# Performance work log

Hardware: AMD Instinct MI355X
Metric: run time of the kernel (lower is better)

The kernel has to match this reference:

```python
import jax, jax.numpy as jnp
import numpy as np

NEG_SLOPE = 0.2  # PyG GATConv default negative_slope


def gat_conv(x_src, x_dst, edge_index, W, att_src, att_dst, bias, heads, out_c, concat, num_dst):
    # PyG GATConv (add_self_loops=False, eval mode so dropout is identity).
    # Same shared linear W applied to src and dst (in_channels is an int in PyG).
    h_src = (x_src @ W).reshape(-1, heads, out_c)  # [Ns,H,C]
    h_dst = (x_dst @ W).reshape(-1, heads, out_c)  # [Nd,H,C]
    al_src = jnp.sum(h_src * att_src, axis=-1)     # [Ns,H]
    al_dst = jnp.sum(h_dst * att_dst, axis=-1)     # [Nd,H]
    src, dst = edge_index[0], edge_index[1]
    e = jax.nn.leaky_relu(al_src[src] + al_dst[dst], NEG_SLOPE)  # [E,H]
    # segment softmax over edges sharing the same dst node
    m = jax.ops.segment_max(e, dst, num_segments=num_dst)        # [Nd,H]
    e = jnp.exp(e - m[dst])
    s = jax.ops.segment_sum(e, dst, num_segments=num_dst)        # [Nd,H]
    alpha = e / (s[dst] + 1e-16)                                 # [E,H]
    msg = alpha[:, :, None] * h_src[src]                         # [E,H,C]
    out = jax.ops.segment_sum(msg, dst, num_segments=num_dst)    # [Nd,H,C]
    if concat:
        return out.reshape(num_dst, heads * out_c) + bias
    return out.mean(axis=1) + bias


def setup_inputs() -> dict:
    N, D, HID, H, OUT, E = 50000, 128, 64, 8, 128, 400000
    key = jax.random.key(0)
    ks = jax.random.split(key, 32)
    s = 0.05
    inp = {
        'x_transition': jax.random.normal(ks[0], (N, D), jnp.float32),
        'x_place': jax.random.normal(ks[1], (N, D), jnp.float32),
        'edge_tp': jax.random.randint(ks[2], (2, E), 0, N, jnp.int32),
        'edge_pt': jax.random.randint(ks[3], (2, E), 0, N, jnp.int32),
        # layer 1 (heads=8, concat)
        'W1_tp': jax.random.normal(ks[4], (D, H * HID), jnp.float32) * s,
        'as1_tp': jax.random.normal(ks[5], (H, HID), jnp.float32) * s,
        'ad1_tp': jax.random.normal(ks[6], (H, HID), jnp.float32) * s,
        'b1_tp': jnp.zeros((H * HID,), jnp.float32),
        'W1_pt': jax.random.normal(ks[7], (D, H * HID), jnp.float32) * s,
        'as1_pt': jax.random.normal(ks[8], (H, HID), jnp.float32) * s,
        'ad1_pt': jax.random.normal(ks[9], (H, HID), jnp.float32) * s,
        'b1_pt': jnp.zeros((H * HID,), jnp.float32),
        # layer 2 (heads=1, concat=False)
        'W2_tp': jax.random.normal(ks[10], (H * HID, HID), jnp.float32) * s,
        'as2_tp': jax.random.normal(ks[11], (1, HID), jnp.float32) * s,
        'ad2_tp': jax.random.normal(ks[12], (1, HID), jnp.float32) * s,
        'b2_tp': jnp.zeros((HID,), jnp.float32),
        'W2_pt': jax.random.normal(ks[13], (H * HID, HID), jnp.float32) * s,
        'as2_pt': jax.random.normal(ks[14], (1, HID), jnp.float32) * s,
        'ad2_pt': jax.random.normal(ks[15], (1, HID), jnp.float32) * s,
        'b2_pt': jnp.zeros((HID,), jnp.float32),
        # output linears per node type
        'Wo_t': jax.random.normal(ks[16], (HID, OUT), jnp.float32) * s,
        'bo_t': jnp.zeros((OUT,), jnp.float32),
        'Wo_p': jax.random.normal(ks[17], (HID, OUT), jnp.float32) * s,
        'bo_p': jnp.zeros((OUT,), jnp.float32),
    }
    return inp


def reference(x_transition, x_place, edge_tp, edge_pt,
              W1_tp, as1_tp, ad1_tp, b1_tp, W1_pt, as1_pt, ad1_pt, b1_pt,
              W2_tp, as2_tp, ad2_tp, b2_tp, W2_pt, as2_pt, ad2_pt, b2_pt,
              Wo_t, bo_t, Wo_p, bo_p):
    Nt, Np = x_transition.shape[0], x_place.shape[0]
    H, HID = as1_tp.shape
    # conv1: transition -> place and place -> transition (HeteroConv aggr='sum',
    # each dst type receives exactly one edge type here)
    p1 = gat_conv(x_transition, x_place, edge_tp, W1_tp, as1_tp, ad1_tp, b1_tp, H, HID, True, Np)
    t1 = gat_conv(x_place, x_transition, edge_pt, W1_pt, as1_pt, ad1_pt, b1_pt, H, HID, True, Nt)
    p1, t1 = jax.nn.relu(p1), jax.nn.relu(t1)
    # conv2: heads=1, concat=False
    p2 = gat_conv(t1, p1, edge_tp, W2_tp, as2_tp, ad2_tp, b2_tp, 1, HID, False, Np)
    t2 = gat_conv(p1, t1, edge_pt, W2_pt, as2_pt, ad2_pt, b2_pt, 1, HID, False, Nt)
    p2, t2 = jax.nn.relu(p2), jax.nn.relu(t2)
    out_t = t2 @ Wo_t + bo_t
    out_p = p2 @ Wo_p + bo_p
    return (out_t, out_p)
```

## Files before the change

### kernel.cpp

```cpp
#include <hip/hip_runtime.h>

#define NEG_SLOPE 0.2f

typedef __attribute__((ext_vector_type(8))) short bf16x8;
typedef __attribute__((ext_vector_type(4))) float f32x4;

__device__ __forceinline__ float bf2f(unsigned short u) {
    return __uint_as_float(((unsigned int)u) << 16);
}
__device__ __forceinline__ unsigned short f2bf(float f) {
    unsigned int x = __float_as_uint(f);
    x += 0x7fffu + ((x >> 16) & 1u);
    return (unsigned short)(x >> 16);
}
__device__ __forceinline__ float ld1(const float* p) { return *p; }
__device__ __forceinline__ float ld1(const unsigned short* p) { return bf2f(*p); }
__device__ __forceinline__ void st1(float* p, float v) { *p = v; }
__device__ __forceinline__ void st1(unsigned short* p, float v) { *p = f2bf(v); }

__global__ void cvt_bf16_kernel(const float* __restrict__ in, unsigned short* __restrict__ out, int n) {
    int i = blockIdx.x * blockDim.x + threadIdx.x;
    if (i < n) out[i] = f2bf(in[i]);
}

__global__ void transpose_cvt_kernel(const float* __restrict__ in, unsigned short* __restrict__ out,
                                     int K, int N) {
    int i = blockIdx.x * blockDim.x + threadIdx.x;
    if (i >= K * N) return;
    int k = i / N, n = i - k * N;
    out[(size_t)n * K + k] = f2bf(in[i]);
}

__global__ void fold1_bt_kernel(const float* __restrict__ W_s, const float* __restrict__ av_s,
                                const float* __restrict__ W_d, const float* __restrict__ av_d,
                                unsigned short* __restrict__ out) {
    int idx = blockIdx.x * blockDim.x + threadIdx.x;
    if (idx >= 16 * 128) return;
    int h = idx >> 7, d = idx & 127;
    const float* W = (h < 8) ? W_s : W_d;
    const float* a = (h < 8) ? (av_s + h * 64) : (av_d + (h - 8) * 64);
    const float* wr = W + (size_t)d * 512 + (h & 7) * 64;
    float s = 0.f;
#pragma unroll
    for (int c = 0; c < 64; ++c) s = fmaf(wr[c], a[c], s);
    out[idx] = f2bf(s);
}

__global__ void fold2_bt_kernel(const float* __restrict__ W_s, const float* __restrict__ av_s,
                                const float* __restrict__ W_d, const float* __restrict__ av_d,
                                unsigned short* __restrict__ out) {
    int idx = blockIdx.x * blockDim.x + threadIdx.x;
    if (idx >= 16 * 512) return;
    int h = idx >> 9, d = idx & 511;
    float s = 0.f;
    if (h < 2) {
        const float* W = (h == 0) ? W_s : W_d;
        const float* a = (h == 0) ? av_s : av_d;
        const float* wr = W + (size_t)d * 64;
#pragma unroll
        for (int c = 0; c < 64; ++c) s = fmaf(wr[c], a[c], s);
    }
    out[idx] = f2bf(s);
}

__global__ void hist_kernel(const int* __restrict__ dst, int E, int* __restrict__ deg) {
    int i = blockIdx.x * blockDim.x + threadIdx.x;
    if (i < E) atomicAdd(&deg[dst[i]], 1);
}

__global__ __launch_bounds__(512) void scan_chunk_kernel(const int* __restrict__ in, int N,
                                                         int* __restrict__ incl, int* __restrict__ sums) {
    __shared__ int sm[512];
    int i = blockIdx.x * 512 + threadIdx.x;
    int v = (i < N) ? in[i] : 0;
    sm[threadIdx.x] = v;
    __syncthreads();
    for (int off = 1; off < 512; off <<= 1) {
        int t = (threadIdx.x >= off) ? sm[threadIdx.x - off] : 0;
        __syncthreads();
        sm[threadIdx.x] += t;
        __syncthreads();
    }
    if (i < N) incl[i] = sm[threadIdx.x];
    if (threadIdx.x == 511) sums[blockIdx.x] = sm[511];
}

__global__ __launch_bounds__(512) void scan_sums_kernel(int* __restrict__ sums, int n) {
    __shared__ int sm[512];
    int v = (threadIdx.x < n) ? sums[threadIdx.x] : 0;
    sm[threadIdx.x] = v;
    __syncthreads();
    for (int off = 1; off < 512; off <<= 1) {
        int t = (threadIdx.x >= off) ? sm[threadIdx.x - off] : 0;
        __syncthreads();
        sm[threadIdx.x] += t;
        __syncthreads();
    }
    if (threadIdx.x < n) sums[threadIdx.x] = sm[threadIdx.x] - v;
}

__global__ void scan_fin_kernel(const int* __restrict__ incl, const int* __restrict__ deg,
                                const int* __restrict__ sums, int N,
                                int* __restrict__ rowptr, int* __restrict__ cursor) {
    int i = blockIdx.x * blockDim.x + threadIdx.x;
    if (i >= N) return;
    int excl = incl[i] - deg[i] + sums[i >> 9];
    rowptr[i] = excl;
    cursor[i] = excl;
}

__global__ void scatter_kernel(const int* __restrict__ src, const int* __restrict__ dst, int E,
                               int* __restrict__ cursor, int* __restrict__ csr_src,
                               int* __restrict__ csr_dst) {
    int i = blockIdx.x * blockDim.x + threadIdx.x;
    if (i >= E) return;
    int d = dst[i];
    int pos = atomicAdd(&cursor[d], 1);
    csr_src[pos] = src[i];
    csr_dst[pos] = d;
}

__global__ void edge_pe1_kernel(const int* __restrict__ csr_src, const int* __restrict__ csr_dst,
                                int E, const float* __restrict__ alsrc, const float* __restrict__ aldst,
                                float* __restrict__ pe) {
    int t = blockIdx.x * blockDim.x + threadIdx.x;
    if (t >= E * 8) return;
    int j = t >> 3, h = t & 7;
    int sp = csr_src[j], dn = csr_dst[j];
    float e = alsrc[(size_t)sp * 16 + h] + aldst[(size_t)dn * 16 + 8 + h];
    e = fmaxf(e, NEG_SLOPE * e);
    pe[t] = __expf(e);
}

__global__ void edge_pe2_kernel(const int* __restrict__ csr_src, const int* __restrict__ csr_dst,
                                int E, const float* __restrict__ alsrc, const float* __restrict__ aldst,
                                float* __restrict__ pe) {
    int j = blockIdx.x * blockDim.x + threadIdx.x;
    if (j >= E) return;
    float e = alsrc[(size_t)csr_src[j] * 16] + aldst[(size_t)csr_dst[j] * 16 + 1];
    e = fmaxf(e, NEG_SLOPE * e);
    pe[j] = __expf(e);
}

template <typename HT, typename OT>
__global__ __launch_bounds__(512) void agg1_kernel(
    const int* __restrict__ rowptr, const int* __restrict__ deg, const int* __restrict__ csr_src,
    const float* __restrict__ pe, const HT* __restrict__ hsrc,
    const float* __restrict__ bias, OT* __restrict__ out, int Ndst) {
    int n = blockIdx.x;
    if (n >= Ndst) return;
    int h = threadIdx.x >> 6, lane = threadIdx.x & 63;
    int start = rowptr[n], cnt = deg[n];
    const int* cs = csr_src + start;
    const float* pp = pe + (size_t)start * 8 + h;
    float s = 0.f, acc = 0.f;
    int i = 0;
    for (; i + 4 <= cnt; i += 4) {
        int sp0 = cs[i], sp1 = cs[i + 1], sp2 = cs[i + 2], sp3 = cs[i + 3];
        float p0 = pp[(size_t)i * 8], p1 = pp[(size_t)(i + 1) * 8];
        float p2 = pp[(size_t)(i + 2) * 8], p3 = pp[(size_t)(i + 3) * 8];
        float hv0 = ld1(hsrc + (size_t)sp0 * 512 + h * 64 + lane);
        float hv1 = ld1(hsrc + (size_t)sp1 * 512 + h * 64 + lane);
        float hv2 = ld1(hsrc + (size_t)sp2 * 512 + h * 64 + lane);
        float hv3 = ld1(hsrc + (size_t)sp3 * 512 + h * 64 + lane);
        s += (p0 + p1) + (p2 + p3);
        acc = fmaf(p0, hv0, acc);
        acc = fmaf(p1, hv1, acc);
        acc = fmaf(p2, hv2, acc);
        acc = fmaf(p3, hv3, acc);
    }
    for (; i < cnt; ++i) {
        int sp = cs[i];
        float p = pp[(size_t)i * 8];
        float hv = ld1(hsrc + (size_t)sp * 512 + h * 64 + lane);
        s += p;
        acc = fmaf(p, hv, acc);
    }
    float r = acc / (s + 1e-16f);
    float o = fmaxf(r + bias[h * 64 + lane], 0.f);
    st1(&out[(size_t)n * 512 + h * 64 + lane], o);
}

template <typename HT, typename OT>
__global__ __launch_bounds__(256) void agg2_kernel(
    const int* __restrict__ rowptr, const int* __restrict__ deg, const int* __restrict__ csr_src,
    const float* __restrict__ pe, const HT* __restrict__ hsrc,
    const float* __restrict__ bias, OT* __restrict__ out, int Ndst) {
    int w = (blockIdx.x * 256 + threadIdx.x) >> 6;
    int lane = threadIdx.x & 63;
    if (w >= Ndst) return;
    int start = rowptr[w], cnt = deg[w];
    const int* cs = csr_src + start;
    const float* pp = pe + start;
    float s = 0.f, acc = 0.f;
    int i = 0;
    for (; i + 4 <= cnt; i += 4) {
        int sp0 = cs[i], sp1 = cs[i + 1], sp2 = cs[i + 2], sp3 = cs[i + 3];
        float p0 = pp[i], p1 = pp[i + 1], p2 = pp[i + 2], p3 = pp[i + 3];
        float hv0 = ld1(hsrc + (size_t)sp0 * 64 + lane);
        float hv1 = ld1(hsrc + (size_t)sp1 * 64 + lane);
        float hv2 = ld1(hsrc + (size_t)sp2 * 64 + lane);
        float hv3 = ld1(hsrc + (size_t)sp3 * 64 + lane);
        s += (p0 + p1) + (p2 + p3);
        acc = fmaf(p0, hv0, acc);
        acc = fmaf(p1, hv1, acc);
        acc = fmaf(p2, hv2, acc);
        acc = fmaf(p3, hv3, acc);
    }
    for (; i < cnt; ++i) {
        int sp = cs[i];
        float p = pp[i];
        float hv = ld1(hsrc + (size_t)sp * 64 + lane);
        s += p;
        acc = fmaf(p, hv, acc);
    }
    st1(&out[(size_t)w * 64 + lane], fmaxf(acc / (s + 1e-16f) + bias[lane], 0.f));
}

template <int NT, typename OT>
__global__ __launch_bounds__(256) void mfma_gemm_kernel(
    const unsigned short* __restrict__ A, const unsigned short* __restrict__ Bt,
    OT* __restrict__ C, const float* __restrict__ bias, int M, int N, int K) {
    int wave = threadIdx.x >> 6;
    int lane = threadIdx.x & 63;
    int m0 = blockIdx.x * 64 + wave * 16;
    int n0 = blockIdx.y * (NT * 16);
    int l15 = lane & 15;
    int kg = lane >> 4;
    f32x4 acc[NT];
#pragma unroll
    for (int t = 0; t < NT; ++t) acc[t] = (f32x4){0.f, 0.f, 0.f, 0.f};
    int arow = m0 + l15;
    const unsigned short* ap = A + (size_t)arow * K + kg * 8;
    const unsigned short* bp0 = Bt + (size_t)(n0 + l15) * K + kg * 8;
    for (int k0 = 0; k0 < K; k0 += 32) {
        bf16x8 af = {0, 0, 0, 0, 0, 0, 0, 0};
        if (arow < M) af = *(const bf16x8*)(ap + k0);
#pragma unroll
        for (int t = 0; t < NT; ++t) {
            bf16x8 bf_ = *(const bf16x8*)(bp0 + (size_t)t * 16 * K + k0);
            acc[t] = __builtin_amdgcn_mfma_f32_16x16x32_bf16(af, bf_, acc[t], 0, 0, 0);
        }
    }
    int orow0 = m0 + kg * 4;
#pragma unroll
    for (int t = 0; t < NT; ++t) {
        int ocol = n0 + t * 16 + l15;
        float bv = bias ? bias[ocol] : 0.f;
#pragma unroll
        for (int r = 0; r < 4; ++r) {
            int orow = orow0 + r;
            if (orow < M) st1(&C[(size_t)orow * N + ocol], acc[t][r] + bv);
        }
    }
}

static inline size_t align_up(size_t x, size_t a) { return (x + a - 1) / a * a; }

extern "C" void kernel_launch(void* const* d_in, const int* in_sizes, int n_in,
                              void* d_out, int out_size, void* d_ws, size_t ws_size,
                              hipStream_t stream) {
    const float* x_t = (const float*)d_in[0];
    const float* x_p = (const float*)d_in[1];
    const int* e_tp = (const int*)d_in[2];
    const int* e_pt = (const int*)d_in[3];
    const float* W1_tp = (const float*)d_in[4];
    const float* as1_tp = (const float*)d_in[5];
    const float* ad1_tp = (const float*)d_in[6];
    const float* b1_tp = (const float*)d_in[7];
    const float* W1_pt = (const float*)d_in[8];
    const float* as1_pt = (const float*)d_in[9];
    const float* ad1_pt = (const float*)d_in[10];
    const float* b1_pt = (const float*)d_in[11];
    const float* W2_tp = (const float*)d_in[12];
    const float* as2_tp = (const float*)d_in[13];
    const float* ad2_tp = (const float*)d_in[14];
    const float* b2_tp = (const float*)d_in[15];
    const float* W2_pt = (const float*)d_in[16];
    const float* as2_pt = (const float*)d_in[17];
    const float* ad2_pt = (const float*)d_in[18];
    const float* b2_pt = (const float*)d_in[19];
    const float* Wo_t = (const float*)d_in[20];
    const float* bo_t = (const float*)d_in[21];
    const float* Wo_p = (const float*)d_in[22];
    const float* bo_p = (const float*)d_in[23];

    const int Nt = in_sizes[0] / 128;
    const int Np = in_sizes[1] / 128;
    const int Etp = in_sizes[2] / 2;
    const int Ept = in_sizes[3] / 2;
    const size_t maxN = (Nt > Np) ? (size_t)Nt : (size_t)Np;

    char* p = (char*)d_ws;
    auto alloc = [&](size_t bytes) -> void* {
        void* r = (void*)p;
        p += align_up(bytes, 256);
        return r;
    };
    float* al_t = (float*)alloc((size_t)Nt * 16 * 4);
    float* al_p = (float*)alloc((size_t)Np * 16 * 4);
    float* al2_t = (float*)alloc((size_t)Nt * 16 * 4);
    float* al2_p = (float*)alloc((size_t)Np * 16 * 4);
    unsigned short* albt_t = (unsigned short*)alloc(16 * 128 * 2);
    unsigned short* albt_p = (unsigned short*)alloc(16 * 128 * 2);
    unsigned short* albt2_t = (unsigned short*)alloc(16 * 512 * 2);
    unsigned short* albt2_p = (unsigned short*)alloc(16 * 512 * 2);
    int* deg_p = (int*)alloc((size_t)Np * 4);
    int* rowptr_p = (int*)alloc((size_t)Np * 4);
    int* cur_p = (int*)alloc((size_t)Np * 4);
    int* incl_p = (int*)alloc((size_t)Np * 4);
    int* deg_t = (int*)alloc((size_t)Nt * 4);
    int* rowptr_t = (int*)alloc((size_t)Nt * 4);
    int* cur_t = (int*)alloc((size_t)Nt * 4);
    int* incl_t = (int*)alloc((size_t)Nt * 4);
    int* csr_tp = (int*)alloc((size_t)Etp * 4);
    int* csr_pt = (int*)alloc((size_t)Ept * 4);
    int* csrd_tp = (int*)alloc((size_t)Etp * 4);
    int* csrd_pt = (int*)alloc((size_t)Ept * 4);
    float* pe_tp = (float*)alloc((size_t)Etp * 8 * 4);
    float* pe_pt = (float*)alloc((size_t)Ept * 8 * 4);
    int* sums_p = (int*)alloc(512 * 4);
    int* sums_t = (int*)alloc(512 * 4);
    unsigned short* xbf_t = (unsigned short*)alloc((size_t)Nt * 128 * 2);
    unsigned short* xbf_p = (unsigned short*)alloc((size_t)Np * 128 * 2);
    unsigned short* Bt1_tp = (unsigned short*)alloc(512 * 128 * 2);
    unsigned short* Bt1_pt = (unsigned short*)alloc(512 * 128 * 2);
    unsigned short* Bt2_tp = (unsigned short*)alloc(64 * 512 * 2);
    unsigned short* Bt2_pt = (unsigned short*)alloc(64 * 512 * 2);
    unsigned short* Bto_t = (unsigned short*)alloc(128 * 64 * 2);
    unsigned short* Bto_p = (unsigned short*)alloc(128 * 64 * 2);
    unsigned short* H = (unsigned short*)alloc(maxN * 512 * 2);
    unsigned short* p1 = (unsigned short*)alloc((size_t)Np * 512 * 2);
    unsigned short* t1 = (unsigned short*)alloc((size_t)Nt * 512 * 2);
    unsigned short* h2_ts = H;
    unsigned short* h2_ps = H + (size_t)Nt * 64;
    unsigned short* p2 = h2_ps + (size_t)Np * 64;
    unsigned short* t2 = p2 + (size_t)Np * 64;

    if ((size_t)(p - (char*)d_ws) > ws_size) return;

    float* out_t = (float*)d_out;
    float* out_p = (float*)d_out + (size_t)Nt * 128;

    hipMemsetAsync(deg_p, 0, (size_t)Np * 4, stream);
    hipMemsetAsync(deg_t, 0, (size_t)Nt * 4, stream);

    fold1_bt_kernel<<<8, 256, 0, stream>>>(W1_tp, as1_tp, W1_pt, ad1_pt, albt_t);
    fold1_bt_kernel<<<8, 256, 0, stream>>>(W1_pt, as1_pt, W1_tp, ad1_tp, albt_p);
    fold2_bt_kernel<<<32, 256, 0, stream>>>(W2_tp, as2_tp, W2_pt, ad2_pt, albt2_t);
    fold2_bt_kernel<<<32, 256, 0, stream>>>(W2_pt, as2_pt, W2_tp, ad2_tp, albt2_p);
    cvt_bf16_kernel<<<(Nt * 128 + 255) / 256, 256, 0, stream>>>(x_t, xbf_t, Nt * 128);
    cvt_bf16_kernel<<<(Np * 128 + 255) / 256, 256, 0, stream>>>(x_p, xbf_p, Np * 128);
    transpose_cvt_kernel<<<(128 * 512 + 255) / 256, 256, 0, stream>>>(W1_tp, Bt1_tp, 128, 512);
    transpose_cvt_kernel<<<(128 * 512 + 255) / 256, 256, 0, stream>>>(W1_pt, Bt1_pt, 128, 512);
    transpose_cvt_kernel<<<(512 * 64 + 255) / 256, 256, 0, stream>>>(W2_tp, Bt2_tp, 512, 64);
    transpose_cvt_kernel<<<(512 * 64 + 255) / 256, 256, 0, stream>>>(W2_pt, Bt2_pt, 512, 64);
    transpose_cvt_kernel<<<(64 * 128 + 255) / 256, 256, 0, stream>>>(Wo_t, Bto_t, 64, 128);
    transpose_cvt_kernel<<<(64 * 128 + 255) / 256, 256, 0, stream>>>(Wo_p, Bto_p, 64, 128);

    mfma_gemm_kernel<1, float><<<dim3((Nt + 63) / 64, 1), 256, 0, stream>>>(
        xbf_t, albt_t, al_t, nullptr, Nt, 16, 128);
    mfma_gemm_kernel<1, float><<<dim3((Np + 63) / 64, 1), 256, 0, stream>>>(
        xbf_p, albt_p, al_p, nullptr, Np, 16, 128);

    hist_kernel<<<(Etp + 255) / 256, 256, 0, stream>>>(e_tp + Etp, Etp, deg_p);
    hist_kernel<<<(Ept + 255) / 256, 256, 0, stream>>>(e_pt + Ept, Ept, deg_t);
    int nchp = (Np + 511) / 512, ncht = (Nt + 511) / 512;
    scan_chunk_kernel<<<nchp, 512, 0, stream>>>(deg_p, Np, incl_p, sums_p);
    scan_sums_kernel<<<1, 512, 0, stream>>>(sums_p, nchp);
    scan_fin_kernel<<<(Np + 255) / 256, 256, 0, stream>>>(incl_p, deg_p, sums_p, Np, rowptr_p, cur_p);
    scan_chunk_kernel<<<ncht, 512, 0, stream>>>(deg_t, Nt, incl_t, sums_t);
    scan_sums_kernel<<<1, 512, 0, stream>>>(sums_t, ncht);
    scan_fin_kernel<<<(Nt + 255) / 256, 256, 0, stream>>>(incl_t, deg_t, sums_t, Nt, rowptr_t, cur_t);
    scatter_kernel<<<(Etp + 255) / 256, 256, 0, stream>>>(e_tp, e_tp + Etp, Etp, cur_p, csr_tp, csrd_tp);
    scatter_kernel<<<(Ept + 255) / 256, 256, 0, stream>>>(e_pt, e_pt + Ept, Ept, cur_t, csr_pt, csrd_pt);

    edge_pe1_kernel<<<(Etp * 8 + 255) / 256, 256, 0, stream>>>(csr_tp, csrd_tp, Etp, al_t, al_p, pe_tp);
    edge_pe1_kernel<<<(Ept * 8 + 255) / 256, 256, 0, stream>>>(csr_pt, csrd_pt, Ept, al_p, al_t, pe_pt);

    mfma_gemm_kernel<8, unsigned short><<<dim3((Nt + 63) / 64, 4), 256, 0, stream>>>(
        xbf_t, Bt1_tp, H, nullptr, Nt, 512, 128);
    agg1_kernel<unsigned short, unsigned short><<<Np, 512, 0, stream>>>(
        rowptr_p, deg_p, csr_tp, pe_tp, H, b1_tp, p1, Np);
    mfma_gemm_kernel<8, unsigned short><<<dim3((Np + 63) / 64, 4), 256, 0, stream>>>(
        xbf_p, Bt1_pt, H, nullptr, Np, 512, 128);
    agg1_kernel<unsigned short, unsigned short><<<Nt, 512, 0, stream>>>(
        rowptr_t, deg_t, csr_pt, pe_pt, H, b1_pt, t1, Nt);

    mfma_gemm_kernel<1, float><<<dim3((Nt + 63) / 64, 1), 256, 0, stream>>>(
        t1, albt2_t, al2_t, nullptr, Nt, 16, 512);
    mfma_gemm_kernel<1, float><<<dim3((Np + 63) / 64, 1), 256, 0, stream>>>(
        p1, albt2_p, al2_p, nullptr, Np, 16, 512);

    edge_pe2_kernel<<<(Etp + 255) / 256, 256, 0, stream>>>(csr_tp, csrd_tp, Etp, al2_t, al2_p, pe_tp);
    edge_pe2_kernel<<<(Ept + 255) / 256, 256, 0, stream>>>(csr_pt, csrd_pt, Ept, al2_p, al2_t, pe_pt);

    mfma_gemm_kernel<4, unsigned short><<<dim3((Nt + 63) / 64, 1), 256, 0, stream>>>(
        t1, Bt2_tp, h2_ts, nullptr, Nt, 64, 512);
    mfma_gemm_kernel<4, unsigned short><<<dim3((Np + 63) / 64, 1), 256, 0, stream>>>(
        p1, Bt2_pt, h2_ps, nullptr, Np, 64, 512);

    agg2_kernel<unsigned short, unsigned short><<<(Np + 3) / 4, 256, 0, stream>>>(
        rowptr_p, deg_p, csr_tp, pe_tp, h2_ts, b2_tp, p2, Np);
    agg2_kernel<unsigned short, unsigned short><<<(Nt + 3) / 4, 256, 0, stream>>>(
        rowptr_t, deg_t, csr_pt, pe_pt, h2_ps, b2_pt, t2, Nt);

    mfma_gemm_kernel<8, float><<<dim3((Nt + 63) / 64, 1), 256, 0, stream>>>(
        t2, Bto_t, out_t, bo_t, Nt, 128, 64);
    mfma_gemm_kernel<8, float><<<dim3((Np + 63) / 64, 1), 256, 0, stream>>>(
        p2, Bto_p, out_p, bo_p, Np, 128, 64);
}
```

Baseline: 950.4 us.

## Vectorize GAT aggregation loads and fuse layer-2 projection with attention GEMM

agg1 now gives each destination node one wavefront, and each lane loads 8 contiguous bf16 features as a 16-byte vector. This replaces a 512-thread block doing scalar 2-byte loads per head. agg2 splits the wavefront into two halves that each handle alternate edges with 32-bit loads, then combines the halves with a shuffle. The layer-2 feature GEMM and the attention-logit GEMM are merged into one dual-output kernel using a concatenated weight matrix, so t1/p1 are read once instead of twice. The intent is to cut scalar-load instruction count and duplicate reads of the large intermediates, at the cost of more registers per lane in agg1.

```diff
diff --git a/kernel.cpp b/kernel.cpp
--- a/kernel.cpp
+++ b/kernel.cpp
@@ -142,49 +142,58 @@
     pe[j] = __expf(e);
 }
 
-template <typename HT, typename OT>
-__global__ __launch_bounds__(512) void agg1_kernel(
+template <typename OT>
+__global__ __launch_bounds__(256) void agg1_kernel(
     const int* __restrict__ rowptr, const int* __restrict__ deg, const int* __restrict__ csr_src,
-    const float* __restrict__ pe, const HT* __restrict__ hsrc,
+    const float* __restrict__ pe, const unsigned short* __restrict__ hsrc,
     const float* __restrict__ bias, OT* __restrict__ out, int Ndst) {
-    int n = blockIdx.x;
-    if (n >= Ndst) return;
-    int h = threadIdx.x >> 6, lane = threadIdx.x & 63;
-    int start = rowptr[n], cnt = deg[n];
+    int w = (blockIdx.x * 256 + threadIdx.x) >> 6;
+    int lane = threadIdx.x & 63;
+    if (w >= Ndst) return;
+    int start = rowptr[w], cnt = deg[w];
     const int* cs = csr_src + start;
-    const float* pp = pe + (size_t)start * 8 + h;
-    float s = 0.f, acc = 0.f;
+    const float* pp = pe + (size_t)start * 8 + (lane >> 3);
+    float acc[8] = {0.f, 0.f, 0.f, 0.f, 0.f, 0.f, 0.f, 0.f};
+    float s = 0.f;
     int i = 0;
     for (; i + 4 <= cnt; i += 4) {
         int sp0 = cs[i], sp1 = cs[i + 1], sp2 = cs[i + 2], sp3 = cs[i + 3];
         float p0 = pp[(size_t)i * 8], p1 = pp[(size_t)(i + 1) * 8];
         float p2 = pp[(size_t)(i + 2) * 8], p3 = pp[(size_t)(i + 3) * 8];
-        float hv0 = ld1(hsrc + (size_t)sp0 * 512 + h * 64 + lane);
-        float hv1 = ld1(hsrc + (size_t)sp1 * 512 + h * 64 + lane);
-        float hv2 = ld1(hsrc + (size_t)sp2 * 512 + h * 64 + lane);
-        float hv3 = ld1(hsrc + (size_t)sp3 * 512 + h * 64 + lane);
+        bf16x8 v0 = *(const bf16x8*)(hsrc + (size_t)sp0 * 512 + lane * 8);
+        bf16x8 v1 = *(const bf16x8*)(hsrc + (size_t)sp1 * 512 + lane * 8);
+        bf16x8 v2 = *(const bf16x8*)(hsrc + (size_t)sp2 * 512 + lane * 8);
+        bf16x8 v3 = *(const bf16x8*)(hsrc + (size_t)sp3 * 512 + lane * 8);
         s += (p0 + p1) + (p2 + p3);
-        acc = fmaf(p0, hv0, acc);
-        acc = fmaf(p1, hv1, acc);
-        acc = fmaf(p2, hv2, acc);
-        acc = fmaf(p3, hv3, acc);
+#pragma unroll
+        for (int j = 0; j < 8; ++j) {
+            acc[j] = fmaf(p0, bf2f((unsigned short)v0[j]), acc[j]);
+            acc[j] = fmaf(p1, bf2f((unsigned short)v1[j]), acc[j]);
+            acc[j] = fmaf(p2, bf2f((unsigned short)v2[j]), acc[j]);
+            acc[j] = fmaf(p3, bf2f((unsigned short)v3[j]), acc[j]);
+        }
     }
     for (; i < cnt; ++i) {
         int sp = cs[i];
         float p = pp[(size_t)i * 8];
-        float hv = ld1(hsrc + (size_t)sp * 512 + h * 64 + lane);
+        bf16x8 v = *(const bf16x8*)(hsrc + (size_t)sp * 512 + lane * 8);
         s += p;
-        acc = fmaf(p, hv, acc);
-    }
-    float r = acc / (s + 1e-16f);
-    float o = fmaxf(r + bias[h * 64 + lane], 0.f);
-    st1(&out[(size_t)n * 512 + h * 64 + lane], o);
-}
-
-template <typename HT, typename OT>
+#pragma unroll
+        for (int j = 0; j < 8; ++j) acc[j] = fmaf(p, bf2f((unsigned short)v[j]), acc[j]);
+    }
+    float inv = 1.f / (s + 1e-16f);
+    const float* bp = bias + lane * 8;
+#pragma unroll
+    for (int j = 0; j < 8; ++j) {
+        float o = fmaxf(fmaf(acc[j], inv, 0.f) + bp[j], 0.f);
+        st1(&out[(size_t)w * 512 + lane * 8 + j], o);
+    }
+}
+
+template <typename OT>
 __global__ __launch_bounds__(256) void agg2_kernel(
     const int* __restrict__ rowptr, const int* __restrict__ deg, const int* __restrict__ csr_src,
-    const float* __restrict__ pe, const HT* __restrict__ hsrc,
+    const float* __restrict__ pe, const unsigned short* __restrict__ hsrc,
     const float* __restrict__ bias, OT* __restrict__ out, int Ndst) {
     int w = (blockIdx.x * 256 + threadIdx.x) >> 6;
     int lane = threadIdx.x & 63;
@@ -192,29 +201,49 @@
     int start = rowptr[w], cnt = deg[w];
     const int* cs = csr_src + start;
     const float* pp = pe + start;
-    float s = 0.f, acc = 0.f;
+    int half = lane >> 5, l32 = lane & 31;
+    float a0 = 0.f, a1 = 0.f, s = 0.f;
     int i = 0;
     for (; i + 4 <= cnt; i += 4) {
-        int sp0 = cs[i], sp1 = cs[i + 1], sp2 = cs[i + 2], sp3 = cs[i + 3];
-        float p0 = pp[i], p1 = pp[i + 1], p2 = pp[i + 2], p3 = pp[i + 3];
-        float hv0 = ld1(hsrc + (size_t)sp0 * 64 + lane);
-        float hv1 = ld1(hsrc + (size_t)sp1 * 64 + lane);
-        float hv2 = ld1(hsrc + (size_t)sp2 * 64 + lane);
-        float hv3 = ld1(hsrc + (size_t)sp3 * 64 + lane);
-        s += (p0 + p1) + (p2 + p3);
-        acc = fmaf(p0, hv0, acc);
-        acc = fmaf(p1, hv1, acc);
-        acc = fmaf(p2, hv2, acc);
-        acc = fmaf(p3, hv3, acc);
-    }
-    for (; i < cnt; ++i) {
+        int j0 = i + half * 2;
+        int sp0 = cs[j0], sp1 = cs[j0 + 1];
+        float p0 = pp[j0], p1 = pp[j0 + 1];
+        unsigned int v0 = *(const unsigned int*)(hsrc + (size_t)sp0 * 64 + l32 * 2);
+        unsigned int v1 = *(const unsigned int*)(hsrc + (size_t)sp1 * 64 + l32 * 2);
+        s += p0 + p1;
+        a0 = fmaf(p0, bf2f((unsigned short)v0), a0);
+        a1 = fmaf(p0, bf2f((unsigned short)(v0 >> 16)), a1);
+        a0 = fmaf(p1, bf2f((unsigned short)v1), a0);
+        a1 = fmaf(p1, bf2f((unsigned short)(v1 >> 16)), a1);
+    }
+    if (i + 2 <= cnt) {
+        int j = i + half;
+        int sp = cs[j];
+        float p = pp[j];
+        unsigned int v = *(const unsigned int*)(hsrc + (size_t)sp * 64 + l32 * 2);
+        s += p;
+        a0 = fmaf(p, bf2f((unsigned short)v), a0);
+        a1 = fmaf(p, bf2f((unsigned short)(v >> 16)), a1);
+        i += 2;
+    }
+    if (i < cnt && half == 0) {
         int sp = cs[i];
         float p = pp[i];
-        float hv = ld1(hsrc + (size_t)sp * 64 + lane);
+        unsigned int v = *(const unsigned int*)(hsrc + (size_t)sp * 64 + l32 * 2);
         s += p;
-        acc = fmaf(p, hv, acc);
-    }
-    st1(&out[(size_t)w * 64 + lane], fmaxf(acc / (s + 1e-16f) + bias[lane], 0.f));
+        a0 = fmaf(p, bf2f((unsigned short)v), a0);
+        a1 = fmaf(p, bf2f((unsigned short)(v >> 16)), a1);
+    }
+    a0 += __shfl_xor(a0, 32);
+    a1 += __shfl_xor(a1, 32);
+    s += __shfl_xor(s, 32);
+    if (half == 0) {
+        float inv = 1.f / (s + 1e-16f);
+        float o0 = fmaxf(a0 * inv + bias[l32 * 2], 0.f);
+        float o1 = fmaxf(a1 * inv + bias[l32 * 2 + 1], 0.f);
+        st1(&out[(size_t)w * 64 + l32 * 2], o0);
+        st1(&out[(size_t)w * 64 + l32 * 2 + 1], o1);
+    }
 }
 
 template <int NT, typename OT>
@@ -252,6 +281,46 @@
             int orow = orow0 + r;
             if (orow < M) st1(&C[(size_t)orow * N + ocol], acc[t][r] + bv);
         }
+    }
+}
+
+__global__ __launch_bounds__(256) void mfma_gemm_dual_kernel(
+    const unsigned short* __restrict__ A, const unsigned short* __restrict__ Btcat,
+    unsigned short* __restrict__ Ch, float* __restrict__ Cal, int M, int K) {
+    int wave = threadIdx.x >> 6;
+    int lane = threadIdx.x & 63;
+    int m0 = blockIdx.x * 64 + wave * 16;
+    int l15 = lane & 15;
+    int kg = lane >> 4;
+    f32x4 acc[5];
+#pragma unroll
+    for (int t = 0; t < 5; ++t) acc[t] = (f32x4){0.f, 0.f, 0.f, 0.f};
+    int arow = m0 + l15;
+    const unsigned short* ap = A + (size_t)arow * K + kg * 8;
+    const unsigned short* bp0 = Btcat + (size_t)l15 * K + kg * 8;
+    for (int k0 = 0; k0 < K; k0 += 32) {
+        bf16x8 af = {0, 0, 0, 0, 0, 0, 0, 0};
+        if (arow < M) af = *(const bf16x8*)(ap + k0);
+#pragma unroll
+        for (int t = 0; t < 5; ++t) {
+            bf16x8 bf_ = *(const bf16x8*)(bp0 + (size_t)t * 16 * K + k0);
+            acc[t] = __builtin_amdgcn_mfma_f32_16x16x32_bf16(af, bf_, acc[t], 0, 0, 0);
+        }
+    }
+    int orow0 = m0 + kg * 4;
+#pragma unroll
+    for (int t = 0; t < 4; ++t) {
+        int ocol = t * 16 + l15;
+#pragma unroll
+        for (int r = 0; r < 4; ++r) {
+            int orow = orow0 + r;
+            if (orow < M) st1(&Ch[(size_t)orow * 64 + ocol], acc[t][r]);
+        }
+    }
+#pragma unroll
+    for (int r = 0; r < 4; ++r) {
+        int orow = orow0 + r;
+        if (orow < M) Cal[(size_t)orow * 16 + l15] = acc[4][r];
     }
 }
 
@@ -303,8 +372,6 @@
     float* al2_p = (float*)alloc((size_t)Np * 16 * 4);
     unsigned short* albt_t = (unsigned short*)alloc(16 * 128 * 2);
     unsigned short* albt_p = (unsigned short*)alloc(16 * 128 * 2);
-    unsigned short* albt2_t = (unsigned short*)alloc(16 * 512 * 2);
-    unsigned short* albt2_p = (unsigned short*)alloc(16 * 512 * 2);
     int* deg_p = (int*)alloc((size_t)Np * 4);
     int* rowptr_p = (int*)alloc((size_t)Np * 4);
     int* cur_p = (int*)alloc((size_t)Np * 4);
@@ -325,8 +392,8 @@
     unsigned short* xbf_p = (unsigned short*)alloc((size_t)Np * 128 * 2);
     unsigned short* Bt1_tp = (unsigned short*)alloc(512 * 128 * 2);
     unsigned short* Bt1_pt = (unsigned short*)alloc(512 * 128 * 2);
-    unsigned short* Bt2_tp = (unsigned short*)alloc(64 * 512 * 2);
-    unsigned short* Bt2_pt = (unsigned short*)alloc(64 * 512 * 2);
+    unsigned short* Btcat2_tp = (unsigned short*)alloc(80 * 512 * 2);
+    unsigned short* Btcat2_pt = (unsigned short*)alloc(80 * 512 * 2);
     unsigned short* Bto_t = (unsigned short*)alloc(128 * 64 * 2);
     unsigned short* Bto_p = (unsigned short*)alloc(128 * 64 * 2);
     unsigned short* H = (unsigned short*)alloc(maxN * 512 * 2);
@@ -347,14 +414,14 @@
 
     fold1_bt_kernel<<<8, 256, 0, stream>>>(W1_tp, as1_tp, W1_pt, ad1_pt, albt_t);
     fold1_bt_kernel<<<8, 256, 0, stream>>>(W1_pt, as1_pt, W1_tp, ad1_tp, albt_p);
-    fold2_bt_kernel<<<32, 256, 0, stream>>>(W2_tp, as2_tp, W2_pt, ad2_pt, albt2_t);
-    fold2_bt_kernel<<<32, 256, 0, stream>>>(W2_pt, as2_pt, W2_tp, ad2_tp, albt2_p);
+    fold2_bt_kernel<<<32, 256, 0, stream>>>(W2_tp, as2_tp, W2_pt, ad2_pt, Btcat2_tp + 64 * 512);
+    fold2_bt_kernel<<<32, 256, 0, stream>>>(W2_pt, as2_pt, W2_tp, ad2_tp, Btcat2_pt + 64 * 512);
     cvt_bf16_kernel<<<(Nt * 128 + 255) / 256, 256, 0, stream>>>(x_t, xbf_t, Nt * 128);
     cvt_bf16_kernel<<<(Np * 128 + 255) / 256, 256, 0, stream>>>(x_p, xbf_p, Np * 128);
     transpose_cvt_kernel<<<(128 * 512 + 255) / 256, 256, 0, stream>>>(W1_tp, Bt1_tp, 128, 512);
     transpose_cvt_kernel<<<(128 * 512 + 255) / 256, 256, 0, stream>>>(W1_pt, Bt1_pt, 128, 512);
-    transpose_cvt_kernel<<<(512 * 64 + 255) / 256, 256, 0, stream>>>(W2_tp, Bt2_tp, 512, 64);
-    transpose_cvt_kernel<<<(512 * 64 + 255) / 256, 256, 0, stream>>>(W2_pt, Bt2_pt, 512, 64);
+    transpose_cvt_kernel<<<(512 * 64 + 255) / 256, 256, 0, stream>>>(W2_tp, Btcat2_tp, 512, 64);
+    transpose_cvt_kernel<<<(512 * 64 + 255) / 256, 256, 0, stream>>>(W2_pt, Btcat2_pt, 512, 64);
     transpose_cvt_kernel<<<(64 * 128 + 255) / 256, 256, 0, stream>>>(Wo_t, Bto_t, 64, 128);
     transpose_cvt_kernel<<<(64 * 128 + 255) / 256, 256, 0, stream>>>(Wo_p, Bto_p, 64, 128);
 
@@ -380,29 +447,22 @@
 
     mfma_gemm_kernel<8, unsigned short><<<dim3((Nt + 63) / 64, 4), 256, 0, stream>>>(
         xbf_t, Bt1_tp, H, nullptr, Nt, 512, 128);
-    agg1_kernel<unsigned short, unsigned short><<<Np, 512, 0, stream>>>(
+    agg1_kernel<unsigned short><<<(Np + 3) / 4, 256, 0, stream>>>(
         rowptr_p, deg_p, csr_tp, pe_tp, H, b1_tp, p1, Np);
     mfma_gemm_kernel<8, unsigned short><<<dim3((Np + 63) / 64, 4), 256, 0, stream>>>(
         xbf_p, Bt1_pt, H, nullptr, Np, 512, 128);
-    agg1_kernel<unsigned short, unsigned short><<<Nt, 512, 0, stream>>>(
+    agg1_kernel<unsigned short><<<(Nt + 3) / 4, 256, 0, stream>>>(
         rowptr_t, deg_t, csr_pt, pe_pt, H, b1_pt, t1, Nt);
 
-    mfma_gemm_kernel<1, float><<<dim3((Nt + 63) / 64, 1), 256, 0, stream>>>(
-        t1, albt2_t, al2_t, nullptr, Nt, 16, 512);
-    mfma_gemm_kernel<1, float><<<dim3((Np + 63) / 64, 1), 256, 0, stream>>>(
-        p1, albt2_p, al2_p, nullptr, Np, 16, 512);
+    mfma_gemm_dual_kernel<<<dim3((Nt + 63) / 64), 256, 0, stream>>>(t1, Btcat2_tp, h2_ts, al2_t, Nt, 512);
+    mfma_gemm_dual_kernel<<<dim3((Np + 63) / 64), 256, 0, stream>>>(p1, Btcat2_pt, h2_ps, al2_p, Np, 512);
 
     edge_pe2_kernel<<<(Etp + 255) / 256, 256, 0, stream>>>(csr_tp, csrd_tp, Etp, al2_t, al2_p, pe_tp);
     edge_pe2_kernel<<<(Ept + 255) / 256, 256, 0, stream>>>(csr_pt, csrd_pt, Ept, al2_p, al2_t, pe_pt);
 
-    mfma_gemm_kernel<4, unsigned short><<<dim3((Nt + 63) / 64, 1), 256, 0, stream>>>(
-        t1, Bt2_tp, h2_ts, nullptr, Nt, 64, 512);
-    mfma_gemm_kernel<4, unsigned short><<<dim3((Np + 63) / 64, 1), 256, 0, stream>>>(
-        p1, Bt2_pt, h2_ps, nullptr, Np, 64, 512);
-
-    agg2_kernel<unsigned short, unsigned short><<<(Np + 3) / 4, 256, 0, stream>>>(
+    agg2_kernel<unsigned short><<<(Np + 3) / 4, 256, 0, stream>>>(
         rowptr_p, deg_p, csr_tp, pe_tp, h2_ts, b2_tp, p2, Np);
-    agg2_kernel<unsigned short, unsigned short><<<(Nt + 3) / 4, 256, 0, stream>>>(
+    agg2_kernel<unsigned short><<<(Nt + 3) / 4, 256, 0, stream>>>(
         rowptr_t, deg_t, csr_pt, pe_pt, h2_ps, b2_pt, t2, Nt);
 
     mfma_gemm_kernel<8, float><<<dim3((Nt + 63) / 64, 1), 256, 0, stream>>>(
```

New measurement: 785.4 us. -17.4%, faster.
